# Kernel tuning notes

Hardware: AMD Instinct MI355X
Metric: run time of the kernel (lower is better)

## Reference

```python
import jax, jax.numpy as jnp
import numpy as np

B, D_IN = 4096, 32000
H0, H1, TAIL = 4000, 4000, 2000
SPARSITY = 0.98


def setup_inputs() -> dict:
    key = jax.random.key(0)
    ks = jax.random.split(key, 8)
    vals = jax.random.normal(ks[0], (B, D_IN), dtype=jnp.float32)
    mask = jax.random.uniform(ks[1], (B, D_IN)) > SPARSITY
    X = vals * mask.astype(jnp.float32)
    def xavier(k, fan_in, fan_out):
        gain = jnp.sqrt(2.0)  # calculate_gain('relu')
        bound = gain * jnp.sqrt(6.0 / (fan_in + fan_out))
        return jax.random.uniform(k, (fan_in, fan_out), dtype=jnp.float32,
                                  minval=-bound, maxval=bound)
    return {
        'X': X,
        'W_in': xavier(ks[2], D_IN, H0), 'b_in': jnp.full((H0,), 0.1, jnp.float32),
        'W1': xavier(ks[3], H0, H1),     'b1': jnp.full((H1,), 0.1, jnp.float32),
        'W2': xavier(ks[4], H1, TAIL),   'b2': jnp.full((TAIL,), 0.1, jnp.float32),
    }


def reference(X, W_in, b_in, W1, b1, W2, b2):
    # SparseLinear: sparse-dense mm + bias (here expressed as dense mm)
    out = jnp.dot(X, W_in) + b_in            # [B, H0]
    # block 0: Linear -> ReLU (dropout identity at eval)
    out = jax.nn.relu(jnp.dot(out, W1) + b1)  # [B, H1]
    # block 1 (tail): Linear -> ReLU
    out = jax.nn.relu(jnp.dot(out, W2) + b2)  # [B, TAIL]
    return out
```

## Files before the change

### kernel.cpp

```cpp
#include <hip/hip_runtime.h>
#include <stdint.h>
#include <stddef.h>


typedef __attribute__((ext_vector_type(8))) short short8;
typedef __attribute__((ext_vector_type(4))) float f32x4;
typedef __attribute__((ext_vector_type(4))) uint32_t u32x4;
typedef __attribute__((ext_vector_type(2))) uint32_t u32x2;

__device__ __forceinline__ uint32_t f2bf_bits(float f) {
  uint32_t u = __builtin_bit_cast(uint32_t, f);
  u += 0x7FFFu + ((u >> 16) & 1u);
  return u >> 16;
}
__device__ __forceinline__ uint32_t pk2(float a, float b) {
  return f2bf_bits(a) | (f2bf_bits(b) << 16);
}

__global__ __launch_bounds__(256)
void cvt_bf16_kernel(const float* __restrict__ in, uint32_t* __restrict__ out, size_t n) {
  size_t i = ((size_t)blockIdx.x * 256 + threadIdx.x) * 8;
  if (i + 8 <= n) {
    f32x4 a = *(const f32x4*)(in + i);
    f32x4 b = *(const f32x4*)(in + i + 4);
    u32x4 o = {pk2(a.x, a.y), pk2(a.z, a.w), pk2(b.x, b.y), pk2(b.z, b.w)};
    *(u32x4*)(out + i / 2) = o;
  }
}

__global__ __launch_bounds__(256)
void cvtT_bf16_kernel(const float* __restrict__ in, uint16_t* __restrict__ out, int K, int N) {
  __shared__ float tile[32][33];
  const int kb = blockIdx.y * 32;
  const int nb = blockIdx.x * 32;
  const int tx = threadIdx.x & 31;
  const int ty = threadIdx.x >> 5;
  const int ncol = nb + tx;
#pragma unroll
  for (int i = 0; i < 32; i += 8)
    tile[ty + i][tx] = (ncol < N) ? in[(size_t)(kb + ty + i) * N + ncol] : 0.f;
  __syncthreads();
#pragma unroll
  for (int i = 0; i < 32; i += 8) {
    int nrow = nb + ty + i;
    if (nrow < N)
      out[(size_t)nrow * K + (kb + tx)] = (uint16_t)f2bf_bits(tile[tx][ty + i]);
  }
}

template<bool ABF16, bool BTBF16, bool RELU, bool OBF16>
__global__ __launch_bounds__(256, 2)
void mlp_gemm(const void* __restrict__ Ap, const void* __restrict__ Bp,
              const float* __restrict__ bias, void* __restrict__ Cp,
              int M, int N, int K)
{
  __shared__ uint16_t As[128][40];
  __shared__ uint16_t Bs[128][40];

  const int tid  = threadIdx.x;
  const int lane = tid & 63;
  const int wave = tid >> 6;
  const int wm = (wave & 1) << 6;
  const int wn = (wave >> 1) << 6;
  const int fl = lane & 15;
  const int kg = lane >> 4;

  const int m0 = blockIdx.y << 7;
  const int n0 = blockIdx.x << 7;

  const int ar = tid >> 1;
  const int ah = (tid & 1) << 4;
  const int bkb = tid >> 5;
  const int bnb = tid & 31;

  const bool n_full = (n0 + 128 <= N);
  const int brow = (n0 + ar < N) ? (n0 + ar) : (N - 1);

  f32x4 acc[4][4];
#pragma unroll
  for (int i = 0; i < 4; ++i)
#pragma unroll
    for (int j = 0; j < 4; ++j)
      acc[i][j] = f32x4{0.f, 0.f, 0.f, 0.f};

  for (int k0 = 0; k0 < K; k0 += 32) {
    {
      u32x4 w0, w1;
      if constexpr (ABF16) {
        const uint16_t* A = (const uint16_t*)Ap;
        const uint16_t* p = A + (size_t)(m0 + ar) * K + (k0 + ah);
        w0 = ((const u32x4*)p)[0];
        w1 = ((const u32x4*)p)[1];
      } else {
        const float* A = (const float*)Ap;
        const float* p = A + (size_t)(m0 + ar) * K + (k0 + ah);
        f32x4 a0 = ((const f32x4*)p)[0];
        f32x4 a1 = ((const f32x4*)p)[1];
        f32x4 a2 = ((const f32x4*)p)[2];
        f32x4 a3 = ((const f32x4*)p)[3];
        w0 = u32x4{pk2(a0.x, a0.y), pk2(a0.z, a0.w), pk2(a1.x, a1.y), pk2(a1.z, a1.w)};
        w1 = u32x4{pk2(a2.x, a2.y), pk2(a2.z, a2.w), pk2(a3.x, a3.y), pk2(a3.z, a3.w)};
      }
      u32x4* d = (u32x4*)&As[ar][ah];
      d[0] = w0; d[1] = w1;
    }
    if constexpr (BTBF16) {
      const uint16_t* Bt = (const uint16_t*)Bp;
      const uint16_t* p = Bt + (size_t)brow * K + (k0 + ah);
      u32x4 w0 = ((const u32x4*)p)[0];
      u32x4 w1 = ((const u32x4*)p)[1];
      u32x4* d = (u32x4*)&Bs[ar][ah];
      d[0] = w0; d[1] = w1;
    } else {
      const float* Bmat = (const float*)Bp;
      if (n_full) {
        const float* p = Bmat + (size_t)(k0 + bkb * 4) * N + (n0 + bnb * 4);
        f32x4 r0 = *(const f32x4*)p;
        f32x4 r1 = *(const f32x4*)(p + (size_t)N);
        f32x4 r2 = *(const f32x4*)(p + 2 * (size_t)N);
        f32x4 r3 = *(const f32x4*)(p + 3 * (size_t)N);
#pragma unroll
        for (int ii = 0; ii < 4; ++ii) {
          u32x2 w = {pk2(r0[ii], r1[ii]), pk2(r2[ii], r3[ii])};
          *(u32x2*)&Bs[bnb * 4 + ii][bkb * 4] = w;
        }
      } else {
#pragma unroll
        for (int ii = 0; ii < 4; ++ii) {
          int n = n0 + bnb * 4 + ii;
          uint32_t b0 = 0, b1 = 0, b2 = 0, b3 = 0;
          if (n < N) {
            size_t o = (size_t)(k0 + bkb * 4) * N + n;
            b0 = f2bf_bits(Bmat[o]);
            b1 = f2bf_bits(Bmat[o + (size_t)N]);
            b2 = f2bf_bits(Bmat[o + 2 * (size_t)N]);
            b3 = f2bf_bits(Bmat[o + 3 * (size_t)N]);
          }
          u32x2 w = {b0 | (b1 << 16), b2 | (b3 << 16)};
          *(u32x2*)&Bs[bnb * 4 + ii][bkb * 4] = w;
        }
      }
    }
    __syncthreads();

    short8 af[4], bfr[4];
#pragma unroll
    for (int t = 0; t < 4; ++t) {
      af[t]  = *(const short8*)&As[wm + t * 16 + fl][kg * 8];
      bfr[t] = *(const short8*)&Bs[wn + t * 16 + fl][kg * 8];
    }
#pragma unroll
    for (int tm = 0; tm < 4; ++tm)
#pragma unroll
      for (int tn = 0; tn < 4; ++tn)
        acc[tm][tn] = __builtin_amdgcn_mfma_f32_16x16x32_bf16(af[tm], bfr[tn], acc[tm][tn], 0, 0, 0);
    __syncthreads();
  }

#pragma unroll
  for (int tn = 0; tn < 4; ++tn) {
    int n = n0 + wn + tn * 16 + fl;
    if (n < N) {
      float bv = bias[n];
#pragma unroll
      for (int tm = 0; tm < 4; ++tm) {
        size_t base = (size_t)(m0 + wm + tm * 16 + kg * 4) * N + n;
#pragma unroll
        for (int r = 0; r < 4; ++r) {
          float v = acc[tm][tn][r] + bv;
          if constexpr (RELU) v = fmaxf(v, 0.f);
          if constexpr (OBF16)
            ((uint16_t*)Cp)[base + (size_t)r * N] = (uint16_t)f2bf_bits(v);
          else
            ((float*)Cp)[base + (size_t)r * N] = v;
        }
      }
    }
  }
}

extern "C" void kernel_launch(void* const* d_in, const int* in_sizes, int n_in,
                              void* d_out, int out_size, void* d_ws, size_t ws_size,
                              hipStream_t stream) {
  const float* X   = (const float*)d_in[0];
  const float* Win = (const float*)d_in[1];
  const float* bin = (const float*)d_in[2];
  const float* W1  = (const float*)d_in[3];
  const float* b1  = (const float*)d_in[4];
  const float* W2  = (const float*)d_in[5];
  const float* b2  = (const float*)d_in[6];
  float* out = (float*)d_out;

  const int Bm = 4096, DIN = 32000, H0 = 4000, H1 = 4000, TL = 2000;
  const size_t sX  = (size_t)Bm * DIN;
  const size_t sWi = (size_t)DIN * H0;
  const size_t sW1 = (size_t)H0 * H1;
  const size_t sW2 = (size_t)H1 * TL;
  const size_t st0 = (size_t)Bm * H0;
  const size_t st1 = (size_t)Bm * H1;
  const size_t need_fast = 2 * (sX + sWi + sW1 + sW2 + st0 + st1);

  dim3 blk(256);

  if (ws_size >= need_fast) {
    uint8_t* w = (uint8_t*)d_ws;
    uint16_t* Xb  = (uint16_t*)w; w += 2 * sX;
    uint16_t* WiT = (uint16_t*)w; w += 2 * sWi;
    uint16_t* W1T = (uint16_t*)w; w += 2 * sW1;
    uint16_t* W2T = (uint16_t*)w; w += 2 * sW2;
    uint16_t* t0  = (uint16_t*)w; w += 2 * st0;
    uint16_t* t1  = (uint16_t*)w;

    cvt_bf16_kernel<<<dim3((unsigned)((sX / 8 + 255) / 256)), blk, 0, stream>>>(X, (uint32_t*)Xb, sX);
    cvtT_bf16_kernel<<<dim3((H0 + 31) / 32, DIN / 32), blk, 0, stream>>>(Win, WiT, DIN, H0);
    cvtT_bf16_kernel<<<dim3((H1 + 31) / 32, H0 / 32), blk, 0, stream>>>(W1, W1T, H0, H1);
    cvtT_bf16_kernel<<<dim3((TL + 31) / 32, H1 / 32), blk, 0, stream>>>(W2, W2T, H1, TL);

    mlp_gemm<true, true, false, true><<<dim3((H0 + 127) / 128, Bm / 128), blk, 0, stream>>>(
        Xb, WiT, bin, t0, Bm, H0, DIN);
    mlp_gemm<true, true, true, true><<<dim3((H1 + 127) / 128, Bm / 128), blk, 0, stream>>>(
        t0, W1T, b1, t1, Bm, H1, H0);
    mlp_gemm<true, true, true, false><<<dim3((TL + 127) / 128, Bm / 128), blk, 0, stream>>>(
        t1, W2T, b2, out, Bm, TL, H1);
  } else {
    uint16_t* t0 = (uint16_t*)d_ws;
    uint16_t* t1 = t0 + st0;

    mlp_gemm<false, false, false, true><<<dim3((H0 + 127) / 128, Bm / 128), blk, 0, stream>>>(
        X, Win, bin, t0, Bm, H0, DIN);
    mlp_gemm<true, false, true, true><<<dim3((H1 + 127) / 128, Bm / 128), blk, 0, stream>>>(
        t0, W1, b1, t1, Bm, H1, H0);
    mlp_gemm<true, false, true, false><<<dim3((TL + 127) / 128, Bm / 128), blk, 0, stream>>>(
        t1, W2, b2, out, Bm, TL, H1);
  }
}
```

Measured before the change: 3.226 ms.

## Use direct global-to-LDS loads with XOR swizzle and grouped tile scheduling

Adds a new bf16 GEMM kernel that loads A and B tiles straight from global memory into LDS with global_load_lds, so data no longer passes through registers. The LDS layout is unpadded and uses an XOR swizzle on 8-element chunks to avoid bank conflicts on the MFMA fragment reads. Workgroup IDs are remapped in groups of eight to improve L2 reuse. The loop is still single-buffered with two barriers per k-step, so load latency is not overlapped with compute.

New measurement: 3.128 ms. 1.03x faster.

```diff
diff --git a/kernel.cpp b/kernel.cpp
--- a/kernel.cpp
+++ b/kernel.cpp
@@ -15,6 +15,12 @@
 }
 __device__ __forceinline__ uint32_t pk2(float a, float b) {
   return f2bf_bits(a) | (f2bf_bits(b) << 16);
+}
+
+__device__ __forceinline__ void gload_lds16(const uint16_t* g, uint16_t* l) {
+  __builtin_amdgcn_global_load_lds(
+      (const __attribute__((address_space(1))) uint32_t*)g,
+      (__attribute__((address_space(3))) uint32_t*)l, 16, 0, 0);
 }
 
 __global__ __launch_bounds__(256)
@@ -45,6 +51,101 @@
     int nrow = nb + ty + i;
     if (nrow < N)
       out[(size_t)nrow * K + (kb + tx)] = (uint16_t)f2bf_bits(tile[tx][ty + i]);
+  }
+}
+
+template<bool RELU, bool OBF16>
+__global__ __launch_bounds__(256, 2)
+void mlp_gemm_fast(const uint16_t* __restrict__ A, const uint16_t* __restrict__ Bt,
+                   const float* __restrict__ bias, void* __restrict__ Cp,
+                   int M, int N, int K)
+{
+  __shared__ uint16_t As[128 * 32];
+  __shared__ uint16_t Bs[128 * 32];
+
+  const int tid  = threadIdx.x;
+  const int lane = tid & 63;
+  const int wave = __builtin_amdgcn_readfirstlane(tid >> 6);
+
+  const int gx = gridDim.x;
+  int nwg = gx * (int)gridDim.y;
+  int wg = (int)blockIdx.y * gx + (int)blockIdx.x;
+  if ((nwg & 7) == 0) { int c = nwg >> 3; wg = (wg & 7) * c + (wg >> 3); }
+  const int n0 = (wg % gx) << 7;
+  const int m0 = (wg / gx) << 7;
+
+  const int wm = (wave & 1) << 6;
+  const int wn = (wave >> 1) << 6;
+  const int fl = lane & 15;
+  const int kg = lane >> 4;
+
+  const int sr = lane >> 2;
+  const int sp = lane & 3;
+  const int r0 = wave * 32 + sr;
+  const int ssw = ((sp ^ ((r0 >> 1) & 3)) << 3);
+
+  const uint16_t* gA0 = A + (size_t)(m0 + r0) * K + ssw;
+  const uint16_t* gA1 = gA0 + (size_t)16 * K;
+  int bn0 = n0 + r0;      if (bn0 > N - 1) bn0 = N - 1;
+  int bn1 = n0 + r0 + 16; if (bn1 > N - 1) bn1 = N - 1;
+  const uint16_t* gB0 = Bt + (size_t)bn0 * K + ssw;
+  const uint16_t* gB1 = Bt + (size_t)bn1 * K + ssw;
+
+  uint16_t* lA0 = &As[wave * 1024];
+  uint16_t* lA1 = lA0 + 512;
+  uint16_t* lB0 = &Bs[wave * 1024];
+  uint16_t* lB1 = lB0 + 512;
+
+  const int colsw = ((kg ^ ((fl >> 1) & 3)) << 3);
+
+  f32x4 acc[4][4];
+#pragma unroll
+  for (int i = 0; i < 4; ++i)
+#pragma unroll
+    for (int j = 0; j < 4; ++j)
+      acc[i][j] = f32x4{0.f, 0.f, 0.f, 0.f};
+
+  for (int k0 = 0; k0 < K; k0 += 32) {
+    gload_lds16(gA0, lA0);
+    gload_lds16(gA1, lA1);
+    gload_lds16(gB0, lB0);
+    gload_lds16(gB1, lB1);
+    gA0 += 32; gA1 += 32; gB0 += 32; gB1 += 32;
+    __syncthreads();
+
+    short8 af[4], bfr[4];
+#pragma unroll
+    for (int t = 0; t < 4; ++t) {
+      af[t]  = *(const short8*)&As[(wm + t * 16 + fl) * 32 + colsw];
+      bfr[t] = *(const short8*)&Bs[(wn + t * 16 + fl) * 32 + colsw];
+    }
+#pragma unroll
+    for (int tm = 0; tm < 4; ++tm)
+#pragma unroll
+      for (int tn = 0; tn < 4; ++tn)
+        acc[tm][tn] = __builtin_amdgcn_mfma_f32_16x16x32_bf16(af[tm], bfr[tn], acc[tm][tn], 0, 0, 0);
+    __syncthreads();
+  }
+
+#pragma unroll
+  for (int tn = 0; tn < 4; ++tn) {
+    int n = n0 + wn + tn * 16 + fl;
+    if (n < N) {
+      float bv = bias[n];
+#pragma unroll
+      for (int tm = 0; tm < 4; ++tm) {
+        size_t base = (size_t)(m0 + wm + tm * 16 + kg * 4) * N + n;
+#pragma unroll
+        for (int r = 0; r < 4; ++r) {
+          float v = acc[tm][tn][r] + bv;
+          if constexpr (RELU) v = fmaxf(v, 0.f);
+          if constexpr (OBF16)
+            ((uint16_t*)Cp)[base + (size_t)r * N] = (uint16_t)f2bf_bits(v);
+          else
+            ((float*)Cp)[base + (size_t)r * N] = v;
+        }
+      }
+    }
   }
 }
 
@@ -216,11 +317,11 @@
     cvtT_bf16_kernel<<<dim3((H1 + 31) / 32, H0 / 32), blk, 0, stream>>>(W1, W1T, H0, H1);
     cvtT_bf16_kernel<<<dim3((TL + 31) / 32, H1 / 32), blk, 0, stream>>>(W2, W2T, H1, TL);
 
-    mlp_gemm<true, true, false, true><<<dim3((H0 + 127) / 128, Bm / 128), blk, 0, stream>>>(
+    mlp_gemm_fast<false, true><<<dim3((H0 + 127) / 128, Bm / 128), blk, 0, stream>>>(
         Xb, WiT, bin, t0, Bm, H0, DIN);
-    mlp_gemm<true, true, true, true><<<dim3((H1 + 127) / 128, Bm / 128), blk, 0, stream>>>(
+    mlp_gemm_fast<true, true><<<dim3((H1 + 127) / 128, Bm / 128), blk, 0, stream>>>(
         t0, W1T, b1, t1, Bm, H1, H0);
-    mlp_gemm<true, true, true, false><<<dim3((TL + 127) / 128, Bm / 128), blk, 0, stream>>>(
+    mlp_gemm_fast<true, false><<<dim3((TL + 127) / 128, Bm / 128), blk, 0, stream>>>(
         t1, W2T, b2, out, Bm, TL, H1);
   } else {
     uint16_t* t0 = (uint16_t*)d_ws;
```
